# Kernel optimization log

Hardware: AMD Instinct MI355X
Metric: run time of the kernel (lower is better)

The kernel has to match this reference:

```python
import jax, jax.numpy as jnp
import numpy as np

P = 920   # spatial positions per frame (hard-coded in source)
FRAMES = 5
H = 8     # num_heads
C = 256   # dim


def setup_inputs() -> dict:
    key = jax.random.key(0)
    ks = jax.random.split(key, 6)
    B = 4
    s = 0.02
    return {
        "x": jax.random.normal(ks[0], (P, B * FRAMES, C), dtype=jnp.float32),
        "W_qkv": jax.random.normal(ks[1], (3 * C, C), dtype=jnp.float32) * s,
        "W_pq": jax.random.normal(ks[2], (C, C), dtype=jnp.float32) * s,
        "W_pkv": jax.random.normal(ks[3], (2 * C, C), dtype=jnp.float32) * s,
        "W_proj": jax.random.normal(ks[4], (C, C), dtype=jnp.float32) * s,
        "b_proj": jnp.zeros((C,), dtype=jnp.float32),
    }


def reference(x, W_qkv, W_pq, W_pkv, W_proj, b_proj):
    d = C // H
    scale = d ** -0.5
    N = FRAMES * P

    # (P, B*F, C) -> (B*F, P, C) -> (B, F*P, C)
    xb = jnp.transpose(x, (1, 0, 2)).reshape(-1, N, C)
    B = xb.shape[0]

    # Stage 1: space attention (note: heads are NOT split here, per original code)
    qkv = xb @ W_qkv.T                      # (B, N, 3C)
    q_, k_, v_ = jnp.split(qkv, 3, axis=-1)
    q_dot_k = jnp.einsum('bqc,bnc->bqn', q_, k_)        # (B, N, N)
    q_dot_k = q_dot_k.reshape(B, N, FRAMES, P)          # b q f n
    space_attn = jax.nn.softmax(scale * q_dot_k, axis=-1)
    v_f = v_.reshape(B, FRAMES, P, C)                   # b f n d
    x1 = jnp.einsum('bqfn,bfnd->bqfd', space_attn, v_f)  # (B, N, F, C)

    # Diagonal extraction: each spatial position attends to its own frame
    xg = x1.reshape(B, FRAMES, P, FRAMES, C)            # b g n f d
    x_diag = jnp.diagonal(xg, axis1=1, axis2=3)         # (B, P, C, F)
    x_diag = jnp.transpose(x_diag, (0, 3, 1, 2)).reshape(B, N, C)  # b (f n) d

    # Stage 2: trajectory attention over frames, with heads
    q2 = x_diag @ W_pq.T                                # (B, N, C)
    kv2 = x1 @ W_pkv.T                                  # (B, N, F, 2C)
    k2, v2 = jnp.split(kv2, 2, axis=-1)
    q2 = q2.reshape(B, N, H, d).transpose(0, 2, 1, 3) * scale      # b h s d
    k2 = k2.reshape(B, N, FRAMES, H, d).transpose(0, 3, 1, 2, 4)   # b h s f d
    v2 = v2.reshape(B, N, FRAMES, H, d).transpose(0, 3, 1, 2, 4)
    attn = jax.nn.softmax(jnp.einsum('bhsd,bhsfd->bhsf', q2, k2), axis=-1)
    x2 = jnp.einsum('bhsf,bhsfd->bhsd', attn, v2)       # (B, H, N, d)
    x2 = x2.transpose(0, 2, 1, 3).reshape(B, N, C)

    out = x2 @ W_proj.T + b_proj                        # (B, N, C)
    out = out.reshape(B, FRAMES, P, C).reshape(B * FRAMES, P, C)
    out = jnp.transpose(out, (1, 0, 2))                 # (P, B*F, C)
    return out, attn
```

## Files before the change

kernel.cpp:

```cpp
#include <hip/hip_runtime.h>
#include <stdint.h>

#define PP 920
#define FF 5
#define BBATCH 4
#define CC 256
#define NN 4600
#define HH 8
#define MROWS 18400
#define M2ROWS 92000
#define SCALE 0.17677669529663687f


typedef short bf16x8 __attribute__((ext_vector_type(8)));
typedef float f32x4 __attribute__((ext_vector_type(4)));
typedef uint32_t u32;

__device__ __forceinline__ float b2f(unsigned short s){
  u32 u = ((u32)s) << 16; float f; __builtin_memcpy(&f, &u, 4); return f;
}
__device__ __forceinline__ unsigned short f2b(float f){
  u32 u; __builtin_memcpy(&u, &f, 4);
  u = (u + 0x7FFFu + ((u >> 16) & 1u)) >> 16;
  return (unsigned short)u;
}


__global__ void k12_cast(const float* __restrict__ in, short* __restrict__ out, int n){
  int i = blockIdx.x*256 + threadIdx.x;
  if (i < n) out[i] = (short)f2b(in[i]);
}

__global__ void k12_make_xb(const float* __restrict__ x, short* __restrict__ xb){
  int i = blockIdx.x*256 + threadIdx.x;
  long e0 = (long)i*4;
  if (e0 >= (long)MROWS*CC) return;
  int row = (int)(e0 >> 8); int c = (int)(e0 & 255);
  int b = row / NN; int s = row - b*NN; int f = s / PP; int p = s - f*PP;
  const float4 v = *(const float4*)(x + ((size_t)(p*(BBATCH*FF) + b*FF + f))*CC + c);
  unsigned short o[4];
  o[0]=f2b(v.x); o[1]=f2b(v.y); o[2]=f2b(v.z); o[3]=f2b(v.w);
  *(ushort4*)(xb + e0) = *(ushort4*)o;
}

__global__ void k12_zero(short* p, int n){
  int i = blockIdx.x*256 + threadIdx.x;
  if (i < n) p[i] = 0;
}

template<int MODE>
__launch_bounds__(256)
__global__ void k12_gemm(const short* __restrict__ A, const short* __restrict__ Bw,
                         short* __restrict__ Cout, float* __restrict__ FCout,
                         const float* __restrict__ bias,
                         int M, int lda, int ldc, float alpha)
{
  __shared__ short As[128][40];
  __shared__ short Bs[128][40];
  const int tid = threadIdx.x;
  const int m0 = blockIdx.x*128, n0 = blockIdx.y*128;
  const int w = tid >> 6, l = tid & 63;
  const int wm = (w >> 1)*64, wn = (w & 1)*64;
  const int lr = l & 15, lg = l >> 4;

  f32x4 acc[4][4] = {};

  for (int k0 = 0; k0 < 256; k0 += 32){
    #pragma unroll
    for (int i = 0; i < 2; i++){
      int v = tid + 256*i;
      int ar = v >> 2, as = (v & 3)*8;
      int grow = m0 + ar; if (grow >= M) grow = M - 1;
      *(uint4*)(&As[ar][as]) = *(const uint4*)(A + (size_t)grow*lda + k0 + as);
      *(uint4*)(&Bs[ar][as]) = *(const uint4*)(Bw + (size_t)(n0 + ar)*256 + k0 + as);
    }
    __syncthreads();
    bf16x8 af[4], bfr[4];
    #pragma unroll
    for (int i = 0; i < 4; i++) af[i]  = *(const bf16x8*)(&As[wm + i*16 + lr][lg*8]);
    #pragma unroll
    for (int j = 0; j < 4; j++) bfr[j] = *(const bf16x8*)(&Bs[wn + j*16 + lr][lg*8]);
    #pragma unroll
    for (int i = 0; i < 4; i++)
      #pragma unroll
      for (int j = 0; j < 4; j++)
        acc[i][j] = __builtin_amdgcn_mfma_f32_16x16x32_bf16(af[i], bfr[j], acc[i][j], 0, 0, 0);
    __syncthreads();
  }

  #pragma unroll
  for (int i = 0; i < 4; i++){
    #pragma unroll
    for (int r = 0; r < 4; r++){
      int m = m0 + wm + i*16 + lg*4 + r;
      if (m >= M) continue;
      #pragma unroll
      for (int j = 0; j < 4; j++){
        int n = n0 + wn + j*16 + lr;
        float v = acc[i][j][r]*alpha;
        if (MODE == 1){
          v += bias[n];
          int b = m / NN, s = m - b*NN; int f = s / PP, p = s - f*PP;
          FCout[(size_t)(p*(BBATCH*FF) + b*FF + f)*CC + n] = v;
        } else {
          Cout[(size_t)m*ldc + n] = (short)f2b(v);
        }
      }
    }
  }
}

__launch_bounds__(256)
__global__ void k12_vt(const short* __restrict__ qkv, short* __restrict__ vt){
  __shared__ short t[64][80];
  const int p0 = blockIdx.x*64;
  const int c0 = blockIdx.y*64;
  const int bf = blockIdx.z;
  const int b = bf / FF, f = bf - b*FF;
  const int tid = threadIdx.x;
  #pragma unroll
  for (int i = 0; i < 2; i++){
    int v = tid + 256*i;
    int pr = v >> 3, sg = (v & 7)*8;
    uint4 val = make_uint4(0,0,0,0);
    int p = p0 + pr;
    if (p < PP)
      val = *(const uint4*)(qkv + ((size_t)(b*NN + f*PP + p))*768 + 512 + c0 + sg);
    *(uint4*)(&t[pr][sg]) = val;
  }
  __syncthreads();
  #pragma unroll
  for (int i = 0; i < 2; i++){
    int v = tid + 256*i;
    int cr = v & 63, pg = v >> 6;
    int pbase = p0 + pg*8;
    if (pbase < 928){
      unsigned short o[8];
      #pragma unroll
      for (int jj = 0; jj < 8; jj++) o[jj] = (unsigned short)t[pg*8 + jj][cr];
      *(uint4*)(vt + ((size_t)(bf*CC + c0 + cr))*928 + pbase) = *(uint4*)o;
    }
  }
}

__launch_bounds__(256)
__global__ void k12_flash(const short* __restrict__ qkv, const short* __restrict__ vt,
                          short* __restrict__ x1, short* __restrict__ xd)
{
  __shared__ short Ks[32][264];
  __shared__ short Vs[256][40];
  __shared__ short Ps[64][32];

  const int qt = blockIdx.x, f = blockIdx.y, b = blockIdx.z;
  const int tid = threadIdx.x, w = tid >> 6, l = tid & 63;
  const int lr = l & 15, lg = l >> 4;
  const int qbase = qt*64;

  bf16x8 qf[8];
  {
    int qrow = qbase + w*16 + lr; if (qrow > NN - 1) qrow = NN - 1;
    const short* qp = qkv + (size_t)(b*NN + qrow)*768;
    #pragma unroll
    for (int kc = 0; kc < 8; kc++) qf[kc] = *(const bf16x8*)(qp + kc*32 + lg*8);
  }

  f32x4 o[16] = {};
  float den[4] = {0.f, 0.f, 0.f, 0.f};

  const size_t krow0 = (size_t)(b*NN + f*PP)*768 + 256;
  const short* vtp = vt + (size_t)((b*FF + f)*CC)*928;

  for (int ch = 0; ch < 29; ch++){
    const int key0 = ch*32;
    #pragma unroll
    for (int i = 0; i < 4; i++){
      int v = tid + 256*i;
      int kr = v >> 5, ks = (v & 31)*8;
      *(uint4*)(&Ks[kr][ks]) = *(const uint4*)(qkv + krow0 + (size_t)(key0 + kr)*768 + ks);
    }
    {
      const short* vp = vtp + (size_t)tid*928 + key0;
      #pragma unroll
      for (int i = 0; i < 4; i++)
        *(uint4*)(&Vs[tid][i*8]) = *(const uint4*)(vp + i*8);
    }
    __syncthreads();

    f32x4 s0 = {}, s1 = {};
    #pragma unroll
    for (int kc = 0; kc < 8; kc++){
      bf16x8 k0v = *(const bf16x8*)(&Ks[lr][kc*32 + lg*8]);
      bf16x8 k1v = *(const bf16x8*)(&Ks[16 + lr][kc*32 + lg*8]);
      s0 = __builtin_amdgcn_mfma_f32_16x16x32_bf16(qf[kc], k0v, s0, 0, 0, 0);
      s1 = __builtin_amdgcn_mfma_f32_16x16x32_bf16(qf[kc], k1v, s1, 0, 0, 0);
    }

    #pragma unroll
    for (int r = 0; r < 4; r++){
      float v0 = s0[r]*SCALE, v1 = s1[r]*SCALE;
      if (key0 + lr      >= PP) v0 = -1e30f;
      if (key0 + 16 + lr >= PP) v1 = -1e30f;
      float p0 = __expf(v0);
      float p1 = __expf(v1);
      den[r] += p0 + p1;
      int qlocal = w*16 + lg*4 + r;
      Ps[qlocal][lr]      = (short)f2b(p0);
      Ps[qlocal][16 + lr] = (short)f2b(p1);
    }
    __syncthreads();

    bf16x8 pa = *(const bf16x8*)(&Ps[w*16 + lr][lg*8]);
    #pragma unroll
    for (int ct = 0; ct < 16; ct++){
      bf16x8 vb = *(const bf16x8*)(&Vs[ct*16 + lr][lg*8]);
      o[ct] = __builtin_amdgcn_mfma_f32_16x16x32_bf16(pa, vb, o[ct], 0, 0, 0);
    }
    __syncthreads();
  }

  #pragma unroll
  for (int r = 0; r < 4; r++){
    float dsum = den[r];
    #pragma unroll
    for (int off = 8; off >= 1; off >>= 1) dsum += __shfl_xor(dsum, off);
    float inv = 1.f/dsum;
    int srow = qbase + w*16 + lg*4 + r;
    if (srow >= NN) continue;
    bool dg = (srow/PP == f);
    size_t x1base = ((size_t)(b*NN + srow)*FF + f)*CC;
    size_t xdbase = (size_t)(b*NN + srow)*CC;
    #pragma unroll
    for (int ct = 0; ct < 16; ct++){
      short val = (short)f2b(o[ct][r]*inv);
      x1[x1base + ct*16 + lr] = val;
      if (dg) xd[xdbase + ct*16 + lr] = val;
    }
  }
}

__launch_bounds__(256)
__global__ void k12_attn2(const short* __restrict__ q2b, const short* __restrict__ k2v2,
                          float* __restrict__ attnp, short* __restrict__ x2)
{
  int idx = blockIdx.x*256 + threadIdx.x;
  if (idx >= MROWS*HH) return;
  const int h = idx & 7; const int row = idx >> 3;

  float qv[32];
  {
    const short* qp = q2b + (size_t)row*CC + h*32;
    #pragma unroll
    for (int s4 = 0; s4 < 4; s4++){
      uint4 u = *(const uint4*)(qp + s4*8);
      const unsigned short* sp = (const unsigned short*)&u;
      #pragma unroll
      for (int j = 0; j < 8; j++) qv[s4*8 + j] = b2f(sp[j]);
    }
  }

  float lgt[FF];
  #pragma unroll
  for (int f = 0; f < FF; f++){
    const short* kp = k2v2 + ((size_t)row*FF + f)*512 + h*32;
    float a = 0.f;
    #pragma unroll
    for (int s4 = 0; s4 < 4; s4++){
      uint4 u = *(const uint4*)(kp + s4*8);
      const unsigned short* sp = (const unsigned short*)&u;
      #pragma unroll
      for (int j = 0; j < 8; j++) a += qv[s4*8 + j]*b2f(sp[j]);
    }
    lgt[f] = a;
  }

  float mx = lgt[0];
  #pragma unroll
  for (int f = 1; f < FF; f++) mx = fmaxf(mx, lgt[f]);
  float pr[FF], ps = 0.f;
  #pragma unroll
  for (int f = 0; f < FF; f++){ pr[f] = __expf(lgt[f] - mx); ps += pr[f]; }
  float inv = 1.f/ps;

  const int b = row / NN; const int s = row - b*NN;
  size_t ab = (((size_t)(b*HH + h))*NN + s)*FF;
  #pragma unroll
  for (int f = 0; f < FF; f++) attnp[ab + f] = pr[f]*inv;

  float xa[32] = {};
  #pragma unroll
  for (int f = 0; f < FF; f++){
    const short* vp = k2v2 + ((size_t)row*FF + f)*512 + 256 + h*32;
    float wgt = pr[f]*inv;
    #pragma unroll
    for (int s4 = 0; s4 < 4; s4++){
      uint4 u = *(const uint4*)(vp + s4*8);
      const unsigned short* sp = (const unsigned short*)&u;
      #pragma unroll
      for (int j = 0; j < 8; j++) xa[s4*8 + j] += wgt*b2f(sp[j]);
    }
  }
  #pragma unroll
  for (int s4 = 0; s4 < 4; s4++){
    unsigned short o[8];
    #pragma unroll
    for (int j = 0; j < 8; j++) o[j] = f2b(xa[s4*8 + j]);
    *(uint4*)(x2 + (size_t)row*CC + h*32 + s4*8) = *(uint4*)o;
  }
}

extern "C" void kernel_launch(void* const* d_in, const int* in_sizes, int n_in,
                              void* d_out, int out_size, void* d_ws, size_t ws_size,
                              hipStream_t stream)
{
  int ix=-1, iwqkv=-1, iwpq=-1, iwpkv=-1, iwproj=-1, ib=-1;
  for (int i = 0; i < n_in; i++){
    switch (in_sizes[i]){
      case 4710400: ix = i; break;
      case 196608:  iwqkv = i; break;
      case 131072:  iwpkv = i; break;
      case 256:     ib = i; break;
      case 65536:   if (iwpq < 0) iwpq = i; else iwproj = i; break;
      default: break;
    }
  }
  if (ix < 0 || iwqkv < 0 || iwpq < 0 || iwpkv < 0 || iwproj < 0 || ib < 0){
    ix=0; iwqkv=1; iwpq=2; iwpkv=3; iwproj=4; ib=5;
  }
  const float* x     = (const float*)d_in[ix];
  const float* Wqkv  = (const float*)d_in[iwqkv];
  const float* Wpq   = (const float*)d_in[iwpq];
  const float* Wpkv  = (const float*)d_in[iwpkv];
  const float* Wproj = (const float*)d_in[iwproj];
  const float* bproj = (const float*)d_in[ib];

  char* ws = (char*)d_ws;
  if (ws_size < 208269312ULL) return;

  short* wq    = (short*)(ws + 0);
  short* wpq   = (short*)(ws + 393216);
  short* wpkv  = (short*)(ws + 524288);
  short* wprj  = (short*)(ws + 786432);
  short* xb    = (short*)(ws + 917504);
  short* qkv   = (short*)(ws + 10338304);
  short* vt    = (short*)(ws + 38612992);
  short* x1    = (short*)(ws + 48115712);
  short* xd    = (short*)(ws + 95219712);
  short* k2v2  = (short*)(ws + 104640512);
  short* q2b   = (short*)(ws + 198848512);
  short* x2    = xb;

  float* outp  = (float*)d_out;
  float* attnp = outp + 4710400;

  k12_cast<<<dim3(768), dim3(256), 0, stream>>>(Wqkv,  wq,   196608);
  k12_cast<<<dim3(256), dim3(256), 0, stream>>>(Wpq,   wpq,  65536);
  k12_cast<<<dim3(512), dim3(256), 0, stream>>>(Wpkv,  wpkv, 131072);
  k12_cast<<<dim3(256), dim3(256), 0, stream>>>(Wproj, wprj, 65536);
  k12_make_xb<<<dim3(4600), dim3(256), 0, stream>>>(x, xb);
  k12_zero<<<dim3(24), dim3(256), 0, stream>>>(qkv + (size_t)MROWS*768, 6144);

  k12_gemm<0><<<dim3(144, 6), dim3(256), 0, stream>>>(xb, wq, qkv, nullptr, nullptr, MROWS, 256, 768, 1.0f);
  k12_vt<<<dim3(15, 4, 20), dim3(256), 0, stream>>>(qkv, vt);
  k12_flash<<<dim3(72, 5, 4), dim3(256), 0, stream>>>(qkv, vt, x1, xd);
  k12_gemm<0><<<dim3(719, 4), dim3(256), 0, stream>>>(x1, wpkv, k2v2, nullptr, nullptr, M2ROWS, 256, 512, 1.0f);
  k12_gemm<0><<<dim3(144, 2), dim3(256), 0, stream>>>(xd, wpq, q2b, nullptr, nullptr, MROWS, 256, 256, SCALE);
  k12_attn2<<<dim3(575), dim3(256), 0, stream>>>(q2b, k2v2, attnp, x2);
  k12_gemm<1><<<dim3(144, 2), dim3(256), 0, stream>>>(x2, wprj, nullptr, outp, bproj, MROWS, 256, 256, 1.0f);
}
```

Baseline: 328.0 us.

## Double query tile per flash block and XOR-swizzle LDS tiles

The space-attention flash kernel now processes 128 query rows per block (two 64-row sub-tiles per wave set), so each K/V chunk loaded into shared memory is reused for twice as many queries and the grid is halved. Shared-memory tiles for K, V and P switch from padded layouts to XOR-swizzled unpadded layouts to avoid bank conflicts, and launch bounds request two blocks per CU. The cost is double the accumulator registers (32 f32x4 output tiles), which risks spills or lower occupancy, and fewer blocks to fill the GPU.

```diff
diff --git a/kernel.cpp b/kernel.cpp
--- a/kernel.cpp
+++ b/kernel.cpp
@@ -16,6 +16,8 @@
 typedef float f32x4 __attribute__((ext_vector_type(4)));
 typedef uint32_t u32;
 
+#define MFMA16 __builtin_amdgcn_mfma_f32_16x16x32_bf16
+
 __device__ __forceinline__ float b2f(unsigned short s){
   u32 u = ((u32)s) << 16; float f; __builtin_memcpy(&f, &u, 4); return f;
 }
@@ -26,12 +28,12 @@
 }
 
 
-__global__ void k12_cast(const float* __restrict__ in, short* __restrict__ out, int n){
+__global__ void k13_cast(const float* __restrict__ in, short* __restrict__ out, int n){
   int i = blockIdx.x*256 + threadIdx.x;
   if (i < n) out[i] = (short)f2b(in[i]);
 }
 
-__global__ void k12_make_xb(const float* __restrict__ x, short* __restrict__ xb){
+__global__ void k13_make_xb(const float* __restrict__ x, short* __restrict__ xb){
   int i = blockIdx.x*256 + threadIdx.x;
   long e0 = (long)i*4;
   if (e0 >= (long)MROWS*CC) return;
@@ -43,14 +45,14 @@
   *(ushort4*)(xb + e0) = *(ushort4*)o;
 }
 
-__global__ void k12_zero(short* p, int n){
+__global__ void k13_zero(short* p, int n){
   int i = blockIdx.x*256 + threadIdx.x;
   if (i < n) p[i] = 0;
 }
 
 template<int MODE>
 __launch_bounds__(256)
-__global__ void k12_gemm(const short* __restrict__ A, const short* __restrict__ Bw,
+__global__ void k13_gemm(const short* __restrict__ A, const short* __restrict__ Bw,
                          short* __restrict__ Cout, float* __restrict__ FCout,
                          const float* __restrict__ bias,
                          int M, int lda, int ldc, float alpha)
@@ -84,7 +86,7 @@
     for (int i = 0; i < 4; i++)
       #pragma unroll
       for (int j = 0; j < 4; j++)
-        acc[i][j] = __builtin_amdgcn_mfma_f32_16x16x32_bf16(af[i], bfr[j], acc[i][j], 0, 0, 0);
+        acc[i][j] = MFMA16(af[i], bfr[j], acc[i][j], 0, 0, 0);
     __syncthreads();
   }
 
@@ -111,7 +113,7 @@
 }
 
 __launch_bounds__(256)
-__global__ void k12_vt(const short* __restrict__ qkv, short* __restrict__ vt){
+__global__ void k13_vt(const short* __restrict__ qkv, short* __restrict__ vt){
   __shared__ short t[64][80];
   const int p0 = blockIdx.x*64;
   const int c0 = blockIdx.y*64;
@@ -143,103 +145,126 @@
   }
 }
 
-__launch_bounds__(256)
-__global__ void k12_flash(const short* __restrict__ qkv, const short* __restrict__ vt,
+__launch_bounds__(256, 2)
+__global__ void k13_flash(const short* __restrict__ qkv, const short* __restrict__ vt,
                           short* __restrict__ x1, short* __restrict__ xd)
 {
-  __shared__ short Ks[32][264];
-  __shared__ short Vs[256][40];
-  __shared__ short Ps[64][32];
+  __shared__ short Ks[32*256];
+  __shared__ short Vs[256*32];
+  __shared__ short Ps[128*32];
 
   const int qt = blockIdx.x, f = blockIdx.y, b = blockIdx.z;
   const int tid = threadIdx.x, w = tid >> 6, l = tid & 63;
   const int lr = l & 15, lg = l >> 4;
-  const int qbase = qt*64;
-
-  bf16x8 qf[8];
-  {
-    int qrow = qbase + w*16 + lr; if (qrow > NN - 1) qrow = NN - 1;
+  const int qbase = qt*128;
+
+  bf16x8 qf[2][8];
+  #pragma unroll
+  for (int t = 0; t < 2; t++){
+    int qrow = qbase + t*64 + w*16 + lr; if (qrow > NN - 1) qrow = NN - 1;
     const short* qp = qkv + (size_t)(b*NN + qrow)*768;
     #pragma unroll
-    for (int kc = 0; kc < 8; kc++) qf[kc] = *(const bf16x8*)(qp + kc*32 + lg*8);
-  }
-
-  f32x4 o[16] = {};
-  float den[4] = {0.f, 0.f, 0.f, 0.f};
+    for (int kc = 0; kc < 8; kc++) qf[t][kc] = *(const bf16x8*)(qp + kc*32 + lg*8);
+  }
+
+  f32x4 o0[16] = {}, o1[16] = {};
+  float den[2][4] = {};
 
   const size_t krow0 = (size_t)(b*NN + f*PP)*768 + 256;
   const short* vtp = vt + (size_t)((b*FF + f)*CC)*928;
 
   for (int ch = 0; ch < 29; ch++){
     const int key0 = ch*32;
+
     #pragma unroll
     for (int i = 0; i < 4; i++){
       int v = tid + 256*i;
-      int kr = v >> 5, ks = (v & 31)*8;
-      *(uint4*)(&Ks[kr][ks]) = *(const uint4*)(qkv + krow0 + (size_t)(key0 + kr)*768 + ks);
+      int kr = v >> 5, s = v & 31;
+      int by = (kr << 9) + (s << 4); by ^= (kr & 7) << 4;
+      *(uint4*)((char*)Ks + by) = *(const uint4*)(qkv + krow0 + (size_t)(key0 + kr)*768 + s*8);
     }
     {
       const short* vp = vtp + (size_t)tid*928 + key0;
       #pragma unroll
-      for (int i = 0; i < 4; i++)
-        *(uint4*)(&Vs[tid][i*8]) = *(const uint4*)(vp + i*8);
-    }
-    __syncthreads();
-
-    f32x4 s0 = {}, s1 = {};
+      for (int i = 0; i < 4; i++){
+        int by = (tid << 6) + (i << 4); by ^= (tid & 7) << 4;
+        *(uint4*)((char*)Vs + by) = *(const uint4*)(vp + i*8);
+      }
+    }
+    __syncthreads();
+
+    f32x4 s00 = {}, s01 = {}, s10 = {}, s11 = {};
     #pragma unroll
     for (int kc = 0; kc < 8; kc++){
-      bf16x8 k0v = *(const bf16x8*)(&Ks[lr][kc*32 + lg*8]);
-      bf16x8 k1v = *(const bf16x8*)(&Ks[16 + lr][kc*32 + lg*8]);
-      s0 = __builtin_amdgcn_mfma_f32_16x16x32_bf16(qf[kc], k0v, s0, 0, 0, 0);
-      s1 = __builtin_amdgcn_mfma_f32_16x16x32_bf16(qf[kc], k1v, s1, 0, 0, 0);
+      int slot = kc*4 + lg;
+      int b0 = (lr << 9)        + (slot << 4); b0 ^= (lr & 7) << 4;
+      int b1 = ((16 + lr) << 9) + (slot << 4); b1 ^= (lr & 7) << 4;
+      bf16x8 k0v = *(const bf16x8*)((char*)Ks + b0);
+      bf16x8 k1v = *(const bf16x8*)((char*)Ks + b1);
+      s00 = MFMA16(qf[0][kc], k0v, s00, 0, 0, 0);
+      s01 = MFMA16(qf[0][kc], k1v, s01, 0, 0, 0);
+      s10 = MFMA16(qf[1][kc], k0v, s10, 0, 0, 0);
+      s11 = MFMA16(qf[1][kc], k1v, s11, 0, 0, 0);
     }
 
     #pragma unroll
     for (int r = 0; r < 4; r++){
-      float v0 = s0[r]*SCALE, v1 = s1[r]*SCALE;
-      if (key0 + lr      >= PP) v0 = -1e30f;
-      if (key0 + 16 + lr >= PP) v1 = -1e30f;
-      float p0 = __expf(v0);
-      float p1 = __expf(v1);
-      den[r] += p0 + p1;
-      int qlocal = w*16 + lg*4 + r;
-      Ps[qlocal][lr]      = (short)f2b(p0);
-      Ps[qlocal][16 + lr] = (short)f2b(p1);
-    }
-    __syncthreads();
-
-    bf16x8 pa = *(const bf16x8*)(&Ps[w*16 + lr][lg*8]);
+      float v00 = s00[r]*SCALE, v01 = s01[r]*SCALE;
+      float v10 = s10[r]*SCALE, v11 = s11[r]*SCALE;
+      if (key0 + lr      >= PP){ v00 = -1e30f; v10 = -1e30f; }
+      if (key0 + 16 + lr >= PP){ v01 = -1e30f; v11 = -1e30f; }
+      float p00 = __expf(v00), p01 = __expf(v01);
+      float p10 = __expf(v10), p11 = __expf(v11);
+      den[0][r] += p00 + p01;
+      den[1][r] += p10 + p11;
+      int q0 = w*16 + lg*4 + r, q1 = 64 + q0;
+      { int by = (q0 << 6) + (lr << 1);        by ^= (q0 & 7) << 4; *(short*)((char*)Ps + by) = (short)f2b(p00); }
+      { int by = (q0 << 6) + ((16 + lr) << 1); by ^= (q0 & 7) << 4; *(short*)((char*)Ps + by) = (short)f2b(p01); }
+      { int by = (q1 << 6) + (lr << 1);        by ^= (q1 & 7) << 4; *(short*)((char*)Ps + by) = (short)f2b(p10); }
+      { int by = (q1 << 6) + ((16 + lr) << 1); by ^= (q1 & 7) << 4; *(short*)((char*)Ps + by) = (short)f2b(p11); }
+    }
+    __syncthreads();
+
+    bf16x8 pa0, pa1;
+    { int r0 = w*16 + lr;      int by = (r0 << 6) + (lg << 4); by ^= (r0 & 7) << 4; pa0 = *(const bf16x8*)((char*)Ps + by); }
+    { int r1 = 64 + w*16 + lr; int by = (r1 << 6) + (lg << 4); by ^= (r1 & 7) << 4; pa1 = *(const bf16x8*)((char*)Ps + by); }
     #pragma unroll
     for (int ct = 0; ct < 16; ct++){
-      bf16x8 vb = *(const bf16x8*)(&Vs[ct*16 + lr][lg*8]);
-      o[ct] = __builtin_amdgcn_mfma_f32_16x16x32_bf16(pa, vb, o[ct], 0, 0, 0);
-    }
-    __syncthreads();
-  }
-
-  #pragma unroll
-  for (int r = 0; r < 4; r++){
-    float dsum = den[r];
-    #pragma unroll
-    for (int off = 8; off >= 1; off >>= 1) dsum += __shfl_xor(dsum, off);
-    float inv = 1.f/dsum;
-    int srow = qbase + w*16 + lg*4 + r;
-    if (srow >= NN) continue;
-    bool dg = (srow/PP == f);
-    size_t x1base = ((size_t)(b*NN + srow)*FF + f)*CC;
-    size_t xdbase = (size_t)(b*NN + srow)*CC;
-    #pragma unroll
-    for (int ct = 0; ct < 16; ct++){
-      short val = (short)f2b(o[ct][r]*inv);
-      x1[x1base + ct*16 + lr] = val;
-      if (dg) xd[xdbase + ct*16 + lr] = val;
+      int vr = ct*16 + lr;
+      int by = (vr << 6) + (lg << 4); by ^= (lr & 7) << 4;
+      bf16x8 vb = *(const bf16x8*)((char*)Vs + by);
+      o0[ct] = MFMA16(pa0, vb, o0[ct], 0, 0, 0);
+      o1[ct] = MFMA16(pa1, vb, o1[ct], 0, 0, 0);
+    }
+    __syncthreads();
+  }
+
+  #pragma unroll
+  for (int t = 0; t < 2; t++){
+    #pragma unroll
+    for (int r = 0; r < 4; r++){
+      float dsum = den[t][r];
+      #pragma unroll
+      for (int off = 8; off >= 1; off >>= 1) dsum += __shfl_xor(dsum, off);
+      float inv = 1.f/dsum;
+      int srow = qbase + t*64 + w*16 + lg*4 + r;
+      if (srow >= NN) continue;
+      bool dg = (srow/PP == f);
+      size_t x1base = ((size_t)(b*NN + srow)*FF + f)*CC;
+      size_t xdbase = (size_t)(b*NN + srow)*CC;
+      #pragma unroll
+      for (int ct = 0; ct < 16; ct++){
+        float ov = t ? o1[ct][r] : o0[ct][r];
+        short val = (short)f2b(ov*inv);
+        x1[x1base + ct*16 + lr] = val;
+        if (dg) xd[xdbase + ct*16 + lr] = val;
+      }
     }
   }
 }
 
 __launch_bounds__(256)
-__global__ void k12_attn2(const short* __restrict__ q2b, const short* __restrict__ k2v2,
+__global__ void k13_attn2(const short* __restrict__ q2b, const short* __restrict__ k2v2,
                           float* __restrict__ attnp, short* __restrict__ x2)
 {
   int idx = blockIdx.x*256 + threadIdx.x;
@@ -352,18 +377,18 @@
   float* outp  = (float*)d_out;
   float* attnp = outp + 4710400;
 
-  k12_cast<<<dim3(768), dim3(256), 0, stream>>>(Wqkv,  wq,   196608);
-  k12_cast<<<dim3(256), dim3(256), 0, stream>>>(Wpq,   wpq,  65536);
-  k12_cast<<<dim3(512), dim3(256), 0, stream>>>(Wpkv,  wpkv, 131072);
-  k12_cast<<<dim3(256), dim3(256), 0, stream>>>(Wproj, wprj, 65536);
-  k12_make_xb<<<dim3(4600), dim3(256), 0, stream>>>(x, xb);
-  k12_zero<<<dim3(24), dim3(256), 0, stream>>>(qkv + (size_t)MROWS*768, 6144);
-
-  k12_gemm<0><<<dim3(144, 6), dim3(256), 0, stream>>>(xb, wq, qkv, nullptr, nullptr, MROWS, 256, 768, 1.0f);
-  k12_vt<<<dim3(15, 4, 20), dim3(256), 0, stream>>>(qkv, vt);
-  k12_flash<<<dim3(72, 5, 4), dim3(256), 0, stream>>>(qkv, vt, x1, xd);
-  k12_gemm<0><<<dim3(719, 4), dim3(256), 0, stream>>>(x1, wpkv, k2v2, nullptr, nullptr, M2ROWS, 256, 512, 1.0f);
-  k12_gemm<0><<<dim3(144, 2), dim3(256), 0, stream>>>(xd, wpq, q2b, nullptr, nullptr, MROWS, 256, 256, SCALE);
-  k12_attn2<<<dim3(575), dim3(256), 0, stream>>>(q2b, k2v2, attnp, x2);
-  k12_gemm<1><<<dim3(144, 2), dim3(256), 0, stream>>>(x2, wprj, nullptr, outp, bproj, MROWS, 256, 256, 1.0f);
-}
+  k13_cast<<<dim3(768), dim3(256), 0, stream>>>(Wqkv,  wq,   196608);
+  k13_cast<<<dim3(256), dim3(256), 0, stream>>>(Wpq,   wpq,  65536);
+  k13_cast<<<dim3(512), dim3(256), 0, stream>>>(Wpkv,  wpkv, 131072);
+  k13_cast<<<dim3(256), dim3(256), 0, stream>>>(Wproj, wprj, 65536);
+  k13_make_xb<<<dim3(4600), dim3(256), 0, stream>>>(x, xb);
+  k13_zero<<<dim3(24), dim3(256), 0, stream>>>(qkv + (size_t)MROWS*768, 6144);
+
+  k13_gemm<0><<<dim3(144, 6), dim3(256), 0, stream>>>(xb, wq, qkv, nullptr, nullptr, MROWS, 256, 768, 1.0f);
+  k13_vt<<<dim3(15, 4, 20), dim3(256), 0, stream>>>(qkv, vt);
+  k13_flash<<<dim3(36, 5, 4), dim3(256), 0, stream>>>(qkv, vt, x1, xd);
+  k13_gemm<0><<<dim3(719, 4), dim3(256), 0, stream>>>(x1, wpkv, k2v2, nullptr, nullptr, M2ROWS, 256, 512, 1.0f);
+  k13_gemm<0><<<dim3(144, 2), dim3(256), 0, stream>>>(xd, wpq, q2b, nullptr, nullptr, MROWS, 256, 256, SCALE);
+  k13_attn2<<<dim3(575), dim3(256), 0, stream>>>(q2b, k2v2, attnp, x2);
+  k13_gemm<1><<<dim3(144, 2), dim3(256), 0, stream>>>(x2, wprj, nullptr, outp, bproj, MROWS, 256, 256, 1.0f);
+}
```

Result: slower. 585.8 us (+78.6%).

## Switch space-attention kernel to 32x32 MFMA with 128-query tiles

Applied to the files above, without the earlier changes.

Rewrites the flash attention kernel to use the 32x32x16 bf16 MFMA instead of 16x16x32, with each wave handling 32 query rows so a block covers 128 queries, and halves the grid. Each K/V chunk staged in shared memory is now reused by twice as many queries, which cuts global and LDS traffic per FLOP. Per-wave P buffers remove one block barrier per chunk. In exchange it raises register pressure (16 Q fragments, 8 f32x16 accumulators, 16 denominators), drops the launch bound, and launches fewer blocks, which risks lower occupancy.

```diff
diff --git a/kernel.cpp b/kernel.cpp
--- a/kernel.cpp
+++ b/kernel.cpp
@@ -14,7 +14,11 @@
 
 typedef short bf16x8 __attribute__((ext_vector_type(8)));
 typedef float f32x4 __attribute__((ext_vector_type(4)));
+typedef float f32x16 __attribute__((ext_vector_type(16)));
 typedef uint32_t u32;
+
+#define MFMA16 __builtin_amdgcn_mfma_f32_16x16x32_bf16
+#define MFMA32 __builtin_amdgcn_mfma_f32_32x32x16_bf16
 
 __device__ __forceinline__ float b2f(unsigned short s){
   u32 u = ((u32)s) << 16; float f; __builtin_memcpy(&f, &u, 4); return f;
@@ -26,12 +30,12 @@
 }
 
 
-__global__ void k12_cast(const float* __restrict__ in, short* __restrict__ out, int n){
+__global__ void k15_cast(const float* __restrict__ in, short* __restrict__ out, int n){
   int i = blockIdx.x*256 + threadIdx.x;
   if (i < n) out[i] = (short)f2b(in[i]);
 }
 
-__global__ void k12_make_xb(const float* __restrict__ x, short* __restrict__ xb){
+__global__ void k15_make_xb(const float* __restrict__ x, short* __restrict__ xb){
   int i = blockIdx.x*256 + threadIdx.x;
   long e0 = (long)i*4;
   if (e0 >= (long)MROWS*CC) return;
@@ -43,14 +47,14 @@
   *(ushort4*)(xb + e0) = *(ushort4*)o;
 }
 
-__global__ void k12_zero(short* p, int n){
+__global__ void k15_zero(short* p, int n){
   int i = blockIdx.x*256 + threadIdx.x;
   if (i < n) p[i] = 0;
 }
 
 template<int MODE>
 __launch_bounds__(256)
-__global__ void k12_gemm(const short* __restrict__ A, const short* __restrict__ Bw,
+__global__ void k15_gemm(const short* __restrict__ A, const short* __restrict__ Bw,
                          short* __restrict__ Cout, float* __restrict__ FCout,
                          const float* __restrict__ bias,
                          int M, int lda, int ldc, float alpha)
@@ -84,7 +88,7 @@
     for (int i = 0; i < 4; i++)
       #pragma unroll
       for (int j = 0; j < 4; j++)
-        acc[i][j] = __builtin_amdgcn_mfma_f32_16x16x32_bf16(af[i], bfr[j], acc[i][j], 0, 0, 0);
+        acc[i][j] = MFMA16(af[i], bfr[j], acc[i][j], 0, 0, 0);
     __syncthreads();
   }
 
@@ -111,7 +115,7 @@
 }
 
 __launch_bounds__(256)
-__global__ void k12_vt(const short* __restrict__ qkv, short* __restrict__ vt){
+__global__ void k15_vt(const short* __restrict__ qkv, short* __restrict__ vt){
   __shared__ short t[64][80];
   const int p0 = blockIdx.x*64;
   const int c0 = blockIdx.y*64;
@@ -143,29 +147,28 @@
   }
 }
 
-__launch_bounds__(256)
-__global__ void k12_flash(const short* __restrict__ qkv, const short* __restrict__ vt,
+__global__ void k15_flash(const short* __restrict__ qkv, const short* __restrict__ vt,
                           short* __restrict__ x1, short* __restrict__ xd)
 {
   __shared__ short Ks[32][264];
   __shared__ short Vs[256][40];
-  __shared__ short Ps[64][32];
+  __shared__ short Ps[4][32][40];
 
   const int qt = blockIdx.x, f = blockIdx.y, b = blockIdx.z;
   const int tid = threadIdx.x, w = tid >> 6, l = tid & 63;
-  const int lr = l & 15, lg = l >> 4;
-  const int qbase = qt*64;
-
-  bf16x8 qf[8];
+  const int cl = l & 31, hi = l >> 5;
+  const int qbase = qt*128 + w*32;
+
+  bf16x8 qa[16];
   {
-    int qrow = qbase + w*16 + lr; if (qrow > NN - 1) qrow = NN - 1;
-    const short* qp = qkv + (size_t)(b*NN + qrow)*768;
-    #pragma unroll
-    for (int kc = 0; kc < 8; kc++) qf[kc] = *(const bf16x8*)(qp + kc*32 + lg*8);
-  }
-
-  f32x4 o[16] = {};
-  float den[4] = {0.f, 0.f, 0.f, 0.f};
+    int qrow = qbase + cl; if (qrow > NN - 1) qrow = NN - 1;
+    const short* qp = qkv + (size_t)(b*NN + qrow)*768 + hi*8;
+    #pragma unroll
+    for (int kk = 0; kk < 16; kk++) qa[kk] = *(const bf16x8*)(qp + kk*16);
+  }
+
+  f32x16 o[8] = {};
+  float den[16] = {};
 
   const size_t krow0 = (size_t)(b*NN + f*PP)*768 + 256;
   const short* vtp = vt + (size_t)((b*FF + f)*CC)*928;
@@ -186,60 +189,57 @@
     }
     __syncthreads();
 
-    f32x4 s0 = {}, s1 = {};
-    #pragma unroll
-    for (int kc = 0; kc < 8; kc++){
-      bf16x8 k0v = *(const bf16x8*)(&Ks[lr][kc*32 + lg*8]);
-      bf16x8 k1v = *(const bf16x8*)(&Ks[16 + lr][kc*32 + lg*8]);
-      s0 = __builtin_amdgcn_mfma_f32_16x16x32_bf16(qf[kc], k0v, s0, 0, 0, 0);
-      s1 = __builtin_amdgcn_mfma_f32_16x16x32_bf16(qf[kc], k1v, s1, 0, 0, 0);
-    }
-
-    #pragma unroll
-    for (int r = 0; r < 4; r++){
-      float v0 = s0[r]*SCALE, v1 = s1[r]*SCALE;
-      if (key0 + lr      >= PP) v0 = -1e30f;
-      if (key0 + 16 + lr >= PP) v1 = -1e30f;
-      float p0 = __expf(v0);
-      float p1 = __expf(v1);
-      den[r] += p0 + p1;
-      int qlocal = w*16 + lg*4 + r;
-      Ps[qlocal][lr]      = (short)f2b(p0);
-      Ps[qlocal][16 + lr] = (short)f2b(p1);
+    f32x16 s = {};
+    #pragma unroll
+    for (int kk = 0; kk < 16; kk++){
+      bf16x8 kb = *(const bf16x8*)(&Ks[cl][kk*16 + hi*8]);
+      s = MFMA32(qa[kk], kb, s, 0, 0, 0);
+    }
+
+    const bool valid = (key0 + cl) < PP;
+    #pragma unroll
+    for (int r = 0; r < 16; r++){
+      float v = valid ? s[r]*SCALE : -1e30f;
+      float p = __expf(v);
+      den[r] += p;
+      int qr = (r & 3) + 8*(r >> 2) + 4*hi;
+      Ps[w][qr][cl] = (short)f2b(p);
+    }
+
+    bf16x8 pa0 = *(const bf16x8*)(&Ps[w][cl][hi*8]);
+    bf16x8 pa1 = *(const bf16x8*)(&Ps[w][cl][16 + hi*8]);
+    #pragma unroll
+    for (int ct = 0; ct < 8; ct++){
+      bf16x8 vb0 = *(const bf16x8*)(&Vs[ct*32 + cl][hi*8]);
+      bf16x8 vb1 = *(const bf16x8*)(&Vs[ct*32 + cl][16 + hi*8]);
+      o[ct] = MFMA32(pa0, vb0, o[ct], 0, 0, 0);
+      o[ct] = MFMA32(pa1, vb1, o[ct], 0, 0, 0);
     }
     __syncthreads();
-
-    bf16x8 pa = *(const bf16x8*)(&Ps[w*16 + lr][lg*8]);
-    #pragma unroll
-    for (int ct = 0; ct < 16; ct++){
-      bf16x8 vb = *(const bf16x8*)(&Vs[ct*16 + lr][lg*8]);
-      o[ct] = __builtin_amdgcn_mfma_f32_16x16x32_bf16(pa, vb, o[ct], 0, 0, 0);
-    }
-    __syncthreads();
-  }
-
-  #pragma unroll
-  for (int r = 0; r < 4; r++){
+  }
+
+  #pragma unroll
+  for (int r = 0; r < 16; r++){
     float dsum = den[r];
     #pragma unroll
-    for (int off = 8; off >= 1; off >>= 1) dsum += __shfl_xor(dsum, off);
+    for (int off = 16; off >= 1; off >>= 1) dsum += __shfl_xor(dsum, off);
     float inv = 1.f/dsum;
-    int srow = qbase + w*16 + lg*4 + r;
+    int srow = qbase + (r & 3) + 8*(r >> 2) + 4*hi;
     if (srow >= NN) continue;
     bool dg = (srow/PP == f);
     size_t x1base = ((size_t)(b*NN + srow)*FF + f)*CC;
     size_t xdbase = (size_t)(b*NN + srow)*CC;
     #pragma unroll
-    for (int ct = 0; ct < 16; ct++){
+    for (int ct = 0; ct < 8; ct++){
       short val = (short)f2b(o[ct][r]*inv);
-      x1[x1base + ct*16 + lr] = val;
-      if (dg) xd[xdbase + ct*16 + lr] = val;
+      x1[x1base + ct*32 + cl] = val;
+      if (dg) xd[xdbase + ct*32 + cl] = val;
     }
   }
 }
 
 __launch_bounds__(256)
-__global__ void k12_attn2(const short* __restrict__ q2b, const short* __restrict__ k2v2,
+__global__ void k15_attn2(const short* __restrict__ q2b, const short* __restrict__ k2v2,
                           float* __restrict__ attnp, short* __restrict__ x2)
 {
   int idx = blockIdx.x*256 + threadIdx.x;
@@ -352,18 +352,18 @@
   float* outp  = (float*)d_out;
   float* attnp = outp + 4710400;
 
-  k12_cast<<<dim3(768), dim3(256), 0, stream>>>(Wqkv,  wq,   196608);
-  k12_cast<<<dim3(256), dim3(256), 0, stream>>>(Wpq,   wpq,  65536);
-  k12_cast<<<dim3(512), dim3(256), 0, stream>>>(Wpkv,  wpkv, 131072);
-  k12_cast<<<dim3(256), dim3(256), 0, stream>>>(Wproj, wprj, 65536);
-  k12_make_xb<<<dim3(4600), dim3(256), 0, stream>>>(x, xb);
-  k12_zero<<<dim3(24), dim3(256), 0, stream>>>(qkv + (size_t)MROWS*768, 6144);
-
-  k12_gemm<0><<<dim3(144, 6), dim3(256), 0, stream>>>(xb, wq, qkv, nullptr, nullptr, MROWS, 256, 768, 1.0f);
-  k12_vt<<<dim3(15, 4, 20), dim3(256), 0, stream>>>(qkv, vt);
-  k12_flash<<<dim3(72, 5, 4), dim3(256), 0, stream>>>(qkv, vt, x1, xd);
-  k12_gemm<0><<<dim3(719, 4), dim3(256), 0, stream>>>(x1, wpkv, k2v2, nullptr, nullptr, M2ROWS, 256, 512, 1.0f);
-  k12_gemm<0><<<dim3(144, 2), dim3(256), 0, stream>>>(xd, wpq, q2b, nullptr, nullptr, MROWS, 256, 256, SCALE);
-  k12_attn2<<<dim3(575), dim3(256), 0, stream>>>(q2b, k2v2, attnp, x2);
-  k12_gemm<1><<<dim3(144, 2), dim3(256), 0, stream>>>(x2, wprj, nullptr, outp, bproj, MROWS, 256, 256, 1.0f);
-}
+  k15_cast<<<dim3(768), dim3(256), 0, stream>>>(Wqkv,  wq,   196608);
+  k15_cast<<<dim3(256), dim3(256), 0, stream>>>(Wpq,   wpq,  65536);
+  k15_cast<<<dim3(512), dim3(256), 0, stream>>>(Wpkv,  wpkv, 131072);
+  k15_cast<<<dim3(256), dim3(256), 0, stream>>>(Wproj, wprj, 65536);
+  k15_make_xb<<<dim3(4600), dim3(256), 0, stream>>>(x, xb);
+  k15_zero<<<dim3(24), dim3(256), 0, stream>>>(qkv + (size_t)MROWS*768, 6144);
+
+  k15_gemm<0><<<dim3(144, 6), dim3(256), 0, stream>>>(xb, wq, qkv, nullptr, nullptr, MROWS, 256, 768, 1.0f);
+  k15_vt<<<dim3(15, 4, 20), dim3(256), 0, stream>>>(qkv, vt);
+  k15_flash<<<dim3(36, 5, 4), dim3(256), 0, stream>>>(qkv, vt, x1, xd);
+  k15_gemm<0><<<dim3(719, 4), dim3(256), 0, stream>>>(x1, wpkv, k2v2, nullptr, nullptr, M2ROWS, 256, 512, 1.0f);
+  k15_gemm<0><<<dim3(144, 2), dim3(256), 0, stream>>>(xd, wpq, q2b, nullptr, nullptr, MROWS, 256, 256, SCALE);
+  k15_attn2<<<dim3(575), dim3(256), 0, stream>>>(q2b, k2v2, attnp, x2);
+  k15_gemm<1><<<dim3(144, 2), dim3(256), 0, stream>>>(x2, wprj, nullptr, outp, bproj, MROWS, 256, 256, 1.0f);
+}
```

Result: slower. 896.6 us (+173.4%).
